# Kernel optimization log

Hardware: AMD Instinct MI355X
Metric: run time of the kernel (lower is better)

The kernel has to match this reference:

```python
import jax, jax.numpy as jnp
import numpy as np

HIDDEN_DIM = 2048
HEAD_NUM = 16
HEAD_DIM = HIDDEN_DIM // HEAD_NUM


def setup_inputs() -> dict:
    key = jax.random.key(0)
    ks = jax.random.split(key, 9)
    B, S, H = 2, 2048, HIDDEN_DIM
    scale = 1.0 / np.sqrt(H)
    X = jax.random.normal(ks[0], (B, S, H), dtype=jnp.float32)
    Wq = jax.random.normal(ks[1], (H, H), dtype=jnp.float32) * scale
    bq = jnp.zeros((H,), dtype=jnp.float32)
    Wk = jax.random.normal(ks[2], (H, H), dtype=jnp.float32) * scale
    bk = jnp.zeros((H,), dtype=jnp.float32)
    Wv = jax.random.normal(ks[3], (H, H), dtype=jnp.float32) * scale
    bv = jnp.zeros((H,), dtype=jnp.float32)
    Wo = jax.random.normal(ks[4], (H, H), dtype=jnp.float32) * scale
    bo = jnp.zeros((H,), dtype=jnp.float32)
    return {"X": X, "Wq": Wq, "bq": bq, "Wk": Wk, "bk": bk,
            "Wv": Wv, "bv": bv, "Wo": Wo, "bo": bo}


def reference(X, Wq, bq, Wk, bk, Wv, bv, Wo, bo):
    B, S, H = X.shape
    # QKV projections (nn.Linear applies x @ W.T + b; weights here stored as [in, out])
    Q = X @ Wq + bq
    K = X @ Wk + bk
    V = X @ Wv + bv
    # [B, heads, S, head_dim]
    q = Q.reshape(B, S, HEAD_NUM, HEAD_DIM).transpose(0, 2, 1, 3)
    k = K.reshape(B, S, HEAD_NUM, HEAD_DIM).transpose(0, 2, 1, 3)
    v = V.reshape(B, S, HEAD_NUM, HEAD_DIM).transpose(0, 2, 1, 3)
    scores = jnp.einsum('bhqd,bhkd->bhqk', q, k) / jnp.sqrt(jnp.float32(HEAD_DIM))
    attn = jax.nn.softmax(scores, axis=-1)  # dropout = identity in eval
    out = jnp.einsum('bhqk,bhkd->bhqd', attn, v)
    out = out.transpose(0, 2, 1, 3).reshape(B, S, H)
    return out @ Wo + bo
```

## Files before the change

kernel.cpp:

```cpp
#include <hip/hip_runtime.h>
#include <hip/hip_bf16.h>
#include <stdint.h>


#define Bc 2
#define Sc 2048
#define Hc 2048
#define NHc 16
#define Dc 128
#define Mc 4096

typedef unsigned short ushortT;
typedef float f32x4 __attribute__((ext_vector_type(4)));
typedef _Float16 f16x8 __attribute__((ext_vector_type(8)));

#define MFMAH(a, b, c) __builtin_amdgcn_mfma_f32_16x16x32_f16((a), (b), (c), 0, 0, 0)
#define MF_AB(a, b, c) MFMAH((a), (b), (c))
#define MF_BA(a, b, c) MFMAH((b), (a), (c))

static __device__ __forceinline__ ushortT f2h(float x) {
    _Float16 h = (_Float16)x;
    return __builtin_bit_cast(unsigned short, h);
}

static __device__ __forceinline__ void load_lds16(const ushortT* g, ushortT* l) {
    __builtin_amdgcn_global_load_lds(
        (__attribute__((address_space(1))) void*)(g),
        (__attribute__((address_space(3))) void*)(l), 16, 0, 0);
}

__global__ __launch_bounds__(256) void pack_a(
    const float* __restrict__ src, ushortT* __restrict__ dst)
{
    const int mt = blockIdx.x, kt = blockIdx.y;
    const int t = threadIdx.x;
    const int kq = t & 15;
    const int r0 = t >> 4;
    ushortT* tile = dst + ((size_t)(mt * 32 + kt)) * 8192;
#pragma unroll
    for (int rr = 0; rr < 8; ++rr) {
        const int row = r0 + rr * 16;
        const float4 v = *(const float4*)(src + (size_t)(mt * 128 + row) * Hc + kt * 64 + kq * 4);
        _Float16 h[4] = {(_Float16)v.x, (_Float16)v.y, (_Float16)v.z, (_Float16)v.w};
        const int gid = kq >> 1, halfg = kq & 1;
        const int gp = gid ^ (row & 7);
        *(uint2*)(tile + (size_t)row * 64 + gp * 8 + halfg * 4) = *(uint2*)h;
    }
}

__global__ __launch_bounds__(256) void pack_b(
    const float* __restrict__ W0, const float* __restrict__ W1,
    const float* __restrict__ W2, const float* __restrict__ W3,
    ushortT* __restrict__ dst)
{
    const int nt = blockIdx.x, kt = blockIdx.y, which = blockIdx.z;
    const float* W = (which == 0) ? W0 : (which == 1) ? W1 : (which == 2) ? W2 : W3;
    const int t = threadIdx.x;
    const int n0 = (t & 31) * 4;
    const int kg = t >> 5;
    ushortT* tile = dst + (size_t)which * 4194304 + ((size_t)(nt * 32 + kt)) * 8192;
    _Float16 h[4][8];
#pragma unroll
    for (int j = 0; j < 8; ++j) {
        const float4 v = *(const float4*)&W[(size_t)(kt * 64 + kg * 8 + j) * Hc + nt * 128 + n0];
        h[0][j] = (_Float16)v.x; h[1][j] = (_Float16)v.y;
        h[2][j] = (_Float16)v.z; h[3][j] = (_Float16)v.w;
    }
#pragma unroll
    for (int i = 0; i < 4; ++i) {
        const int n = n0 + i;
        *(uint4*)(tile + (size_t)n * 64 + ((kg ^ (n & 7)) << 3)) = *(uint4*)h[i];
    }
}

#define GEMM_PROLOGUE()                                                        \
    __shared__ __align__(16) ushortT As[8192], Bs[8192];                       \
    const int tid = threadIdx.x, wv_ = tid >> 6, lane = tid & 63;              \
    const int lane16 = lane & 15, quad = lane >> 4;                            \
    const int quad4 = quad * 4;                                                \
    const int wm = (wv_ & 1) * 64, wn = (wv_ >> 1) * 64;                       \
    int aoff[4][2], boff[4][2];                                                \
    _Pragma("unroll") for (int mi = 0; mi < 4; ++mi)                           \
        _Pragma("unroll") for (int kf = 0; kf < 2; ++kf) {                     \
            const int ra = wm + mi * 16 + lane16;                              \
            aoff[mi][kf] = ra * 64 + (((kf * 4 + quad) ^ (ra & 7)) << 3);      \
            const int rb = wn + mi * 16 + lane16;                              \
            boff[mi][kf] = rb * 64 + (((kf * 4 + quad) ^ (rb & 7)) << 3);      \
        }                                                                      \
    f32x4 acc[4][4];                                                           \
    _Pragma("unroll") for (int i = 0; i < 4; ++i)                              \
        _Pragma("unroll") for (int j = 0; j < 4; ++j) {                        \
            acc[i][j][0] = 0.f; acc[i][j][1] = 0.f;                            \
            acc[i][j][2] = 0.f; acc[i][j][3] = 0.f; }                          \
    ushortT* asd = &As[wv_ * 2048];                                            \
    ushortT* bsd = &Bs[wv_ * 2048];

#define GEMM_KLOOP(at, bt, MF)                                                 \
    for (int kt2 = 0; kt2 < 32; ++kt2) {                                       \
        _Pragma("unroll") for (int i = 0; i < 4; ++i) {                        \
            load_lds16(at + i * 512 + lane * 8, asd + i * 512);                \
            load_lds16(bt + i * 512 + lane * 8, bsd + i * 512);                \
        }                                                                      \
        at += 8192; bt += 8192;                                                \
        __syncthreads();                                                       \
        _Pragma("unroll") for (int kf = 0; kf < 2; ++kf) {                     \
            f16x8 a[4], b[4];                                                  \
            _Pragma("unroll") for (int mi = 0; mi < 4; ++mi)                   \
                a[mi] = *(const f16x8*)&As[aoff[mi][kf]];                      \
            _Pragma("unroll") for (int nj = 0; nj < 4; ++nj)                   \
                b[nj] = *(const f16x8*)&Bs[boff[nj][kf]];                      \
            _Pragma("unroll") for (int nj = 0; nj < 4; ++nj)                   \
                _Pragma("unroll") for (int mi = 0; mi < 4; ++mi)               \
                    acc[mi][nj] = MF(a[mi], b[nj], acc[mi][nj]);               \
        }                                                                      \
        __syncthreads();                                                       \
    }

#define G256_PROLOGUE()                                                        \
    __shared__ __align__(16) ushortT LA[2][2][8192];                           \
    __shared__ __align__(16) ushortT LB[2][2][8192];                           \
    const int tid = threadIdx.x, wv_ = tid >> 6, lane = tid & 63;              \
    const int lane16 = lane & 15, quad = lane >> 4, quad4 = (lane >> 4) * 4;   \
    const int wr = wv_ >> 2, wc = wv_ & 3;                                     \
    const ushortT* LAr = &LA[0][0][0] + wr * 8192;                             \
    const ushortT* LBr = &LB[0][0][0] + (wc >> 1) * 8192;                      \
    int oA[2][4][2], oB[4][2];                                                 \
    _Pragma("unroll") for (int h = 0; h < 2; ++h)                              \
        _Pragma("unroll") for (int mi = 0; mi < 4; ++mi)                       \
            _Pragma("unroll") for (int kf = 0; kf < 2; ++kf) {                 \
                const int r_ = h * 64 + mi * 16 + lane16;                      \
                oA[h][mi][kf] = r_ * 64 + (((kf * 4 + quad) ^ (r_ & 7)) << 3); \
            }                                                                  \
    _Pragma("unroll") for (int nj = 0; nj < 4; ++nj)                           \
        _Pragma("unroll") for (int kf = 0; kf < 2; ++kf) {                     \
            const int r_ = (wc & 1) * 64 + nj * 16 + lane16;                   \
            oB[nj][kf] = r_ * 64 + (((kf * 4 + quad) ^ (r_ & 7)) << 3);        \
        }                                                                      \
    f32x4 acc[8][4];                                                           \
    _Pragma("unroll") for (int i = 0; i < 8; ++i)                              \
        _Pragma("unroll") for (int j = 0; j < 4; ++j) {                        \
            acc[i][j][0] = 0.f; acc[i][j][1] = 0.f;                            \
            acc[i][j][2] = 0.f; acc[i][j][3] = 0.f; }

#define STAGE(SRC, STEP, DST) do {                                             \
    const ushortT* g_ = (SRC) + (size_t)(STEP) * 8192;                         \
    ushortT* l_ = (DST) + wv_ * 1024;                                          \
    load_lds16(g_, l_);                                                        \
    load_lds16(g_ + 512, l_ + 512);                                            \
} while (0)

#define RD_A03(S)                                                              \
    _Pragma("unroll") for (int mi = 0; mi < 4; ++mi)                           \
        _Pragma("unroll") for (int kf = 0; kf < 2; ++kf)                       \
            a03[mi][kf] = *(const f16x8*)&LAr[(S) * 16384 + oA[0][mi][kf]];

#define RD_A47(S)                                                              \
    _Pragma("unroll") for (int mi = 0; mi < 4; ++mi)                           \
        _Pragma("unroll") for (int kf = 0; kf < 2; ++kf)                       \
            a47[mi][kf] = *(const f16x8*)&LAr[(S) * 16384 + oA[1][mi][kf]];

#define RD_B01(S)                                                              \
    _Pragma("unroll") for (int nj = 0; nj < 2; ++nj)                           \
        _Pragma("unroll") for (int kf = 0; kf < 2; ++kf)                       \
            b[nj][kf] = *(const f16x8*)&LBr[(S) * 16384 + oB[nj][kf]];

#define RD_B23(S)                                                              \
    _Pragma("unroll") for (int nj = 2; nj < 4; ++nj)                           \
        _Pragma("unroll") for (int kf = 0; kf < 2; ++kf)                       \
            b[nj][kf] = *(const f16x8*)&LBr[(S) * 16384 + oB[nj][kf]];

#define QUADQ(ARR, MIB, NJB, MF)                                               \
    _Pragma("unroll") for (int kf = 0; kf < 2; ++kf)                           \
        _Pragma("unroll") for (int mi = 0; mi < 4; ++mi)                       \
            _Pragma("unroll") for (int nj = 0; nj < 2; ++nj)                   \
                acc[(MIB) + mi][(NJB) + nj] =                                  \
                    MF(ARR[mi][kf], b[(NJB) + nj][kf], acc[(MIB) + mi][(NJB) + nj]);

#define PRE_MFMA()                                                             \
    __builtin_amdgcn_s_barrier();                                              \
    __builtin_amdgcn_s_setprio(1);

#define POST_MFMA()                                                            \
    __builtin_amdgcn_s_setprio(0);                                             \
    __builtin_amdgcn_s_barrier();

#define VMC6() asm volatile("s_waitcnt vmcnt(6)" ::: "memory")
#define VMC4() asm volatile("s_waitcnt vmcnt(4)" ::: "memory")

#define MINS(x) ((x) < 31 ? (x) : 31)

#define G256_MAIN(AB0, AB1, BB0, BB1, MF)                                      \
    const ushortT* sA0 = (AB0) + wv_ * 1024 + lane * 8;                        \
    const ushortT* sA1 = (AB1) + wv_ * 1024 + lane * 8;                        \
    const ushortT* sB0 = (BB0) + wv_ * 1024 + lane * 8;                        \
    const ushortT* sB1 = (BB1) + wv_ * 1024 + lane * 8;                        \
      \
    STAGE(sB0, 0, &LB[0][0][0]); STAGE(sB1, 0, &LB[0][1][0]);                  \
    STAGE(sA0, 0, &LA[0][0][0]); STAGE(sA1, 0, &LA[0][1][0]);                  \
    STAGE(sB0, 1, &LB[1][0][0]); STAGE(sB1, 1, &LB[1][1][0]);                  \
    STAGE(sA0, 1, &LA[1][0][0]);                                               \
    VMC6();                                                                    \
    __builtin_amdgcn_s_barrier();                                              \
    _Pragma("clang loop unroll(disable)")                                      \
    for (int t = 0; t < 32; t += 2) {                                          \
        f16x8 a03[4][2], a47[4][2], b[4][2];                                   \
                                        \
        RD_A03(0); RD_B01(0);                                                  \
        STAGE(sA1, t + 1, &LA[1][1][0]);                                       \
        PRE_MFMA(); QUADQ(a03, 0, 0, MF); POST_MFMA();                         \
                                                       \
        RD_B23(0);                                                             \
        PRE_MFMA(); QUADQ(a03, 0, 2, MF); POST_MFMA();                         \
                             \
        RD_A47(0);                                                             \
        STAGE(sB0, MINS(t + 2), &LB[0][0][0]);                                 \
        PRE_MFMA(); QUADQ(a47, 4, 2, MF); POST_MFMA();                         \
              \
        STAGE(sB1, MINS(t + 2), &LB[0][1][0]);                                 \
        VMC4();                                                                \
        PRE_MFMA(); QUADQ(a47, 4, 0, MF); POST_MFMA();                         \
                        \
        RD_A03(1); RD_B01(1);                                                  \
        STAGE(sA0, MINS(t + 2), &LA[0][0][0]);                                 \
        STAGE(sA1, MINS(t + 2), &LA[0][1][0]);                                 \
        PRE_MFMA(); QUADQ(a03, 0, 0, MF); POST_MFMA();                         \
                                                                       \
        RD_B23(1);                                                             \
        PRE_MFMA(); QUADQ(a03, 0, 2, MF); POST_MFMA();                         \
                                                                       \
        RD_A47(1);                                                             \
        STAGE(sB0, MINS(t + 3), &LB[1][0][0]);                                 \
        PRE_MFMA(); QUADQ(a47, 4, 2, MF); POST_MFMA();                         \
        \
        STAGE(sB1, MINS(t + 3), &LB[1][1][0]);                                 \
        STAGE(sA0, MINS(t + 3), &LA[1][0][0]);                                 \
        VMC6();                                                                \
        PRE_MFMA(); QUADQ(a47, 4, 0, MF); POST_MFMA();                         \
    }

__global__ __launch_bounds__(512, 2) void qkv_gemm256(
    const ushortT* __restrict__ Xp, const ushortT* __restrict__ Wall,
    const float* __restrict__ bq, const float* __restrict__ bk,
    const float* __restrict__ bv,
    ushortT* __restrict__ Qd, ushortT* __restrict__ Kd, ushortT* __restrict__ Vt)
{
    const int id = blockIdx.x;
    const int swz = (id & 7) * 48 + (id >> 3);
    const int mt = swz & 15;
    const int bn = swz >> 4;
    const int which = bn >> 3, bnw = bn & 7;
    const ushortT* Ab0 = Xp + (size_t)((2 * mt + 0) * 32) * 8192;
    const ushortT* Ab1 = Xp + (size_t)((2 * mt + 1) * 32) * 8192;
    const ushortT* Wp  = Wall + (size_t)which * 4194304;
    const ushortT* Bb0 = Wp + (size_t)((bnw * 2 + 0) * 32) * 8192;
    const ushortT* Bb1 = Wp + (size_t)((bnw * 2 + 1) * 32) * 8192;
    const float* bias = (which == 0) ? bq : (which == 1) ? bk : bv;

    G256_PROLOGUE();

    const float QS = 0.08838834764831845f * 1.4426950408889634f;

    if (which == 2) {
        G256_MAIN(Ab0, Ab1, Bb0, Bb1, MF_AB);
        asm volatile("s_waitcnt vmcnt(0)" ::: "memory");
#pragma unroll
        for (int nj = 0; nj < 4; ++nj) {
            const int colm = bnw * 256 + wc * 64 + nj * 16 + lane16;
            const float bb2 = bias[colm];
            const int dd = colm & 127;
            const int hh = colm >> 7;
#pragma unroll
            for (int mi = 0; mi < 8; ++mi) {
                const int m0 = mt * 256 + wr * 128 + mi * 16 + quad4;
                const int b = m0 >> 11, s0_ = m0 & 2047;
                const size_t bhb = (size_t)(b * NHc + hh) * (Sc * Dc);
                const int t2 = s0_ >> 6, sin0 = s0_ & 63;
                uint2 u;
                u.x = (uint32_t)f2h(acc[mi][nj][0] + bb2) |
                      ((uint32_t)f2h(acc[mi][nj][1] + bb2) << 16);
                u.y = (uint32_t)f2h(acc[mi][nj][2] + bb2) |
                      ((uint32_t)f2h(acc[mi][nj][3] + bb2) << 16);
                *(uint2*)&Vt[bhb + (size_t)t2 * 8192 + dd * 64 +
                             (((sin0 >> 3) ^ (dd & 7)) << 3) + (sin0 & 7)] = u;
            }
        }
    } else {
        G256_MAIN(Ab0, Ab1, Bb0, Bb1, MF_BA);
        asm volatile("s_waitcnt vmcnt(0)" ::: "memory");
#pragma unroll
        for (int nj = 0; nj < 4; ++nj) {
            const int col0 = bnw * 256 + wc * 64 + nj * 16 + quad4;
            const float4 bv4 = *(const float4*)&bias[col0];
            const int dd0 = col0 & 127;
            const int hh = col0 >> 7;
#pragma unroll
            for (int mi = 0; mi < 8; ++mi) {
                const int m = mt * 256 + wr * 128 + mi * 16 + lane16;
                const int b = m >> 11, s = m & 2047;
                const size_t bhb = (size_t)(b * NHc + hh) * (Sc * Dc);
                float v0 = acc[mi][nj][0] + bv4.x;
                float v1 = acc[mi][nj][1] + bv4.y;
                float v2 = acc[mi][nj][2] + bv4.z;
                float v3 = acc[mi][nj][3] + bv4.w;
                if (which == 0) {
                    uint2 u;
                    u.x = (uint32_t)f2h(v0 * QS) | ((uint32_t)f2h(v1 * QS) << 16);
                    u.y = (uint32_t)f2h(v2 * QS) | ((uint32_t)f2h(v3 * QS) << 16);
                    *(uint2*)&Qd[bhb + (size_t)s * Dc + dd0] = u;
                } else {
                    const int t2 = s >> 6, sin_ = s & 63;
                    uint2 u;
                    u.x = (uint32_t)f2h(v0) | ((uint32_t)f2h(v1) << 16);
                    u.y = (uint32_t)f2h(v2) | ((uint32_t)f2h(v3) << 16);
                    *(uint2*)&Kd[bhb + (size_t)t2 * 8192 + sin_ * 128 +
                                 (((dd0 >> 3) ^ (sin_ & 7)) << 3) + (dd0 & 7)] = u;
                }
            }
        }
    }
}

__global__ __launch_bounds__(128, 2) void attn(
    const ushortT* __restrict__ Qd, const ushortT* __restrict__ Kt,
    const ushortT* __restrict__ Vt, ushortT* __restrict__ AOp)
{
    const int id = blockIdx.x;
    const int slot = id >> 3;
    const int pair = (id & 7) + ((slot >> 5) << 3);
    const int qt = slot & 31;
    const int hh = pair & 15, bb = pair >> 4;

    const ushortT* Qp  = Qd + ((size_t)(bb * NHc + hh)) * Sc * Dc;
    const ushortT* Kbh = Kt + ((size_t)(bb * NHc + hh)) * Sc * Dc;
    const ushortT* Vbh = Vt + ((size_t)(bb * NHc + hh)) * Sc * Dc;

    __shared__ __align__(16) ushortT Ks[8192];
    __shared__ __align__(16) ushortT Vs[8192];
    __shared__ __align__(16) ushortT Pbuf[2][2048];

    const int tid = threadIdx.x, wv_ = tid >> 6, lane = tid & 63;
    const int lane16 = lane & 15, quad = lane >> 4;
    const int quad8 = quad * 8, quad4 = quad * 4;
    const int s0 = qt * 64 + wv_ * 32;

    f16x8 q[2][4];
#pragma unroll
    for (int nj = 0; nj < 2; ++nj)
#pragma unroll
        for (int kf = 0; kf < 4; ++kf)
            q[nj][kf] = *(const f16x8*)(Qp + (size_t)(s0 + nj * 16 + lane16) * Dc + kf * 32 + quad8);

    f32x4 o[8][2];
#pragma unroll
    for (int dj = 0; dj < 8; ++dj)
#pragma unroll
        for (int nj = 0; nj < 2; ++nj) { o[dj][nj][0] = 0.f; o[dj][nj][1] = 0.f; o[dj][nj][2] = 0.f; o[dj][nj][3] = 0.f; }

    float m_run[2] = {-1e30f, -1e30f}, l_run[2] = {0.f, 0.f};
    ushortT* Pw = Pbuf[wv_];

    for (int nt = 0; nt < 32; ++nt) {
        const ushortT* ktile = Kbh + (size_t)nt * 8192 + wv_ * 4096;
        const ushortT* vtile = Vbh + (size_t)nt * 8192 + wv_ * 4096;
#pragma unroll
        for (int i = 0; i < 8; ++i) {
            load_lds16(ktile + i * 512 + lane * 8, Ks + wv_ * 4096 + i * 512);
            load_lds16(vtile + i * 512 + lane * 8, Vs + wv_ * 4096 + i * 512);
        }
        __syncthreads();

        f32x4 sacc[4][2];
#pragma unroll
        for (int mi = 0; mi < 4; ++mi)
#pragma unroll
            for (int nj = 0; nj < 2; ++nj) { sacc[mi][nj][0] = 0.f; sacc[mi][nj][1] = 0.f; sacc[mi][nj][2] = 0.f; sacc[mi][nj][3] = 0.f; }
        __builtin_amdgcn_s_setprio(1);
#pragma unroll
        for (int kf = 0; kf < 4; ++kf) {
            f16x8 kb[4];
#pragma unroll
            for (int mi = 0; mi < 4; ++mi) {
                const int row = mi * 16 + lane16;
                kb[mi] = *(const f16x8*)&Ks[row * 128 + (((kf * 4 + quad) ^ (row & 7)) << 3)];
            }
#pragma unroll
            for (int mi = 0; mi < 4; ++mi)
#pragma unroll
                for (int nj = 0; nj < 2; ++nj)
                    sacc[mi][nj] = MFMAH(kb[mi], q[nj][kf], sacc[mi][nj]);
        }
        __builtin_amdgcn_s_setprio(0);

        float alpha_[2];
#pragma unroll
        for (int nj = 0; nj < 2; ++nj) {
            float mx = sacc[0][nj][0];
#pragma unroll
            for (int mi = 0; mi < 4; ++mi)
#pragma unroll
                for (int r = 0; r < 4; ++r) mx = fmaxf(mx, sacc[mi][nj][r]);
            mx = fmaxf(mx, __shfl_xor(mx, 16));
            mx = fmaxf(mx, __shfl_xor(mx, 32));
            const float mnew = fmaxf(m_run[nj], mx);
            alpha_[nj] = exp2f(m_run[nj] - mnew);
            m_run[nj] = mnew;
            float sum = 0.f;
#pragma unroll
            for (int mi = 0; mi < 4; ++mi)
#pragma unroll
                for (int r = 0; r < 4; ++r) {
                    const float p = exp2f(sacc[mi][nj][r] - mnew);
                    sacc[mi][nj][r] = p;
                    sum += p;
                }
            sum += __shfl_xor(sum, 16);
            sum += __shfl_xor(sum, 32);
            l_run[nj] = l_run[nj] * alpha_[nj] + sum;
            const int prow = nj * 16 + lane16;
#pragma unroll
            for (int mi = 0; mi < 4; ++mi) {
                uint2 u;
                u.x = (uint32_t)f2h(sacc[mi][nj][0]) | ((uint32_t)f2h(sacc[mi][nj][1]) << 16);
                u.y = (uint32_t)f2h(sacc[mi][nj][2]) | ((uint32_t)f2h(sacc[mi][nj][3]) << 16);
                const int g = mi * 2 + (quad >> 1);
                *(uint2*)&Pw[prow * 64 + ((g ^ (prow & 7)) << 3) + (quad & 1) * 4] = u;
            }
        }

        if (__ballot((alpha_[0] != 1.f) | (alpha_[1] != 1.f)) != 0ull) {
#pragma unroll
            for (int dj = 0; dj < 8; ++dj)
#pragma unroll
                for (int nj = 0; nj < 2; ++nj) {
                    const float av = alpha_[nj];
                    o[dj][nj][0] *= av; o[dj][nj][1] *= av;
                    o[dj][nj][2] *= av; o[dj][nj][3] *= av;
                }
        }

        __builtin_amdgcn_s_setprio(1);
#pragma unroll
        for (int kf2 = 0; kf2 < 2; ++kf2) {
            f16x8 pb[2];
#pragma unroll
            for (int nj = 0; nj < 2; ++nj) {
                const int row = nj * 16 + lane16;
                pb[nj] = *(const f16x8*)&Pw[row * 64 + (((kf2 * 4 + quad) ^ (row & 7)) << 3)];
            }
#pragma unroll
            for (int dj = 0; dj < 8; ++dj) {
                const int row = dj * 16 + lane16;
                const f16x8 vb = *(const f16x8*)&Vs[row * 64 + (((kf2 * 4 + quad) ^ (row & 7)) << 3)];
#pragma unroll
                for (int nj = 0; nj < 2; ++nj)
                    o[dj][nj] = MFMAH(vb, pb[nj], o[dj][nj]);
            }
        }
        __builtin_amdgcn_s_setprio(0);
        __syncthreads();
    }

#pragma unroll
    for (int nj = 0; nj < 2; ++nj) {
        const float inv = 1.f / l_run[nj];
        const int m = bb * Sc + qt * 64 + wv_ * 32 + nj * 16 + lane16;
        const int mtile = m >> 7, rin = m & 127;
#pragma unroll
        for (int dj = 0; dj < 8; ++dj) {
            const int ktile = hh * 2 + (dj >> 2);
            const int cin0 = (dj & 3) * 16 + quad4;
            const int g = cin0 >> 3, e0 = cin0 & 7;
            uint2 u;
            u.x = (uint32_t)f2h(o[dj][nj][0] * inv) | ((uint32_t)f2h(o[dj][nj][1] * inv) << 16);
            u.y = (uint32_t)f2h(o[dj][nj][2] * inv) | ((uint32_t)f2h(o[dj][nj][3] * inv) << 16);
            *(uint2*)&AOp[((size_t)(mtile * 32 + ktile)) * 8192 + rin * 64 +
                          ((g ^ (rin & 7)) << 3) + e0] = u;
        }
    }
}

__global__ __launch_bounds__(256) void out_gemm(
    const ushortT* __restrict__ AOp, const ushortT* __restrict__ Wop,
    const float* __restrict__ bo, float* __restrict__ out)
{
    const int nt = blockIdx.x;
    const int mt = blockIdx.y;

    GEMM_PROLOGUE();

    const ushortT* at = AOp + (size_t)(mt * 32) * 8192 + wv_ * 2048;
    const ushortT* bt = Wop + (size_t)(nt * 32) * 8192 + wv_ * 2048;
    GEMM_KLOOP(at, bt, MF_BA);

#pragma unroll
    for (int nj = 0; nj < 4; ++nj) {
        const int col0 = nt * 128 + wn + nj * 16 + quad4;
        const float4 bv4 = *(const float4*)&bo[col0];
#pragma unroll
        for (int mi = 0; mi < 4; ++mi) {
            const int m = mt * 128 + wm + mi * 16 + lane16;
            float4 v;
            v.x = acc[mi][nj][0] + bv4.x;
            v.y = acc[mi][nj][1] + bv4.y;
            v.z = acc[mi][nj][2] + bv4.z;
            v.w = acc[mi][nj][3] + bv4.w;
            *(float4*)&out[(size_t)m * Hc + col0] = v;
        }
    }
}

extern "C" void kernel_launch(void* const* d_in, const int* in_sizes, int n_in,
                              void* d_out, int out_size, void* d_ws, size_t ws_size,
                              hipStream_t stream) {
    (void)in_sizes; (void)n_in; (void)out_size; (void)ws_size;

    const float* X  = (const float*)d_in[0];
    const float* Wq = (const float*)d_in[1];
    const float* bq = (const float*)d_in[2];
    const float* Wk = (const float*)d_in[3];
    const float* bk = (const float*)d_in[4];
    const float* Wv = (const float*)d_in[5];
    const float* bv = (const float*)d_in[6];
    const float* Wo = (const float*)d_in[7];
    const float* bo = (const float*)d_in[8];
    float* out = (float*)d_out;

    ushortT* ws = (ushortT*)d_ws;
    const size_t E = (size_t)Mc * Hc;
    const size_t WE = (size_t)Hc * Hc;
    ushortT* Xp   = ws;
    ushortT* Wall = Xp + E;
    ushortT* Qd   = Wall + 4 * WE;
    ushortT* Kd   = Qd + E;
    ushortT* Vtp  = Kd + E;
    ushortT* AOp  = Vtp + E;

    pack_a<<<dim3(32, 32), 256, 0, stream>>>(X, Xp);
    pack_b<<<dim3(16, 32, 4), 256, 0, stream>>>(Wq, Wk, Wv, Wo, Wall);
    qkv_gemm256<<<dim3(384), 512, 0, stream>>>(Xp, Wall, bq, bk, bv, Qd, Kd, Vtp);
    attn<<<dim3(1024), 128, 0, stream>>>(Qd, Kd, Vtp, AOp);
    out_gemm<<<dim3(16, 32), 256, 0, stream>>>(AOp, Wall + 3 * WE, bo, out);
}
```

Measured before the change: 430.2 us.

## Double-buffer K/V tiles in attention and widen blocks to 128 queries

The attention kernel now runs 4 waves (256 threads) per block covering 128 query rows, so each K/V tile staged in LDS is shared by twice as many queries. K/V tiles are double-buffered, with the next tile prefetched while the current one is computed on, to hide global-to-LDS latency. The grid is halved and the block-to-XCD mapping is changed so each XCD handles a group of heads. LDS use roughly doubles (about 80KB per block), which may limit how many blocks fit per CU.

```diff
diff --git a/kernel.cpp b/kernel.cpp
--- a/kernel.cpp
+++ b/kernel.cpp
@@ -194,7 +194,6 @@
     const ushortT* sA1 = (AB1) + wv_ * 1024 + lane * 8;                        \
     const ushortT* sB0 = (BB0) + wv_ * 1024 + lane * 8;                        \
     const ushortT* sB1 = (BB1) + wv_ * 1024 + lane * 8;                        \
-      \
     STAGE(sB0, 0, &LB[0][0][0]); STAGE(sB1, 0, &LB[0][1][0]);                  \
     STAGE(sA0, 0, &LA[0][0][0]); STAGE(sA1, 0, &LA[0][1][0]);                  \
     STAGE(sB0, 1, &LB[1][0][0]); STAGE(sB1, 1, &LB[1][1][0]);                  \
@@ -211,15 +210,15 @@
                                                        \
         RD_B23(0);                                                             \
         PRE_MFMA(); QUADQ(a03, 0, 2, MF); POST_MFMA();                         \
-                             \
+                                                       \
         RD_A47(0);                                                             \
         STAGE(sB0, MINS(t + 2), &LB[0][0][0]);                                 \
         PRE_MFMA(); QUADQ(a47, 4, 2, MF); POST_MFMA();                         \
-              \
+                              \
         STAGE(sB1, MINS(t + 2), &LB[0][1][0]);                                 \
         VMC4();                                                                \
         PRE_MFMA(); QUADQ(a47, 4, 0, MF); POST_MFMA();                         \
-                        \
+                                                     \
         RD_A03(1); RD_B01(1);                                                  \
         STAGE(sA0, MINS(t + 2), &LA[0][0][0]);                                 \
         STAGE(sA1, MINS(t + 2), &LA[0][1][0]);                                 \
@@ -231,7 +230,7 @@
         RD_A47(1);                                                             \
         STAGE(sB0, MINS(t + 3), &LB[1][0][0]);                                 \
         PRE_MFMA(); QUADQ(a47, 4, 2, MF); POST_MFMA();                         \
-        \
+                          \
         STAGE(sB1, MINS(t + 3), &LB[1][1][0]);                                 \
         STAGE(sA0, MINS(t + 3), &LA[1][0][0]);                                 \
         VMC6();                                                                \
@@ -320,28 +319,29 @@
     }
 }
 
-__global__ __launch_bounds__(128, 2) void attn(
+__global__ __launch_bounds__(256, 2) void attn(
     const ushortT* __restrict__ Qd, const ushortT* __restrict__ Kt,
     const ushortT* __restrict__ Vt, ushortT* __restrict__ AOp)
 {
     const int id = blockIdx.x;
-    const int slot = id >> 3;
-    const int pair = (id & 7) + ((slot >> 5) << 3);
-    const int qt = slot & 31;
+    const int xcd = id & 7;
+    const int idx = id >> 3;
+    const int pair = (xcd << 2) | (idx >> 4);
+    const int qt = idx & 15;
     const int hh = pair & 15, bb = pair >> 4;
 
     const ushortT* Qp  = Qd + ((size_t)(bb * NHc + hh)) * Sc * Dc;
     const ushortT* Kbh = Kt + ((size_t)(bb * NHc + hh)) * Sc * Dc;
     const ushortT* Vbh = Vt + ((size_t)(bb * NHc + hh)) * Sc * Dc;
 
-    __shared__ __align__(16) ushortT Ks[8192];
-    __shared__ __align__(16) ushortT Vs[8192];
-    __shared__ __align__(16) ushortT Pbuf[2][2048];
+    __shared__ __align__(16) ushortT Ks[2][8192];
+    __shared__ __align__(16) ushortT Vs[2][8192];
+    __shared__ __align__(16) ushortT Pbuf[4][2048];
 
     const int tid = threadIdx.x, wv_ = tid >> 6, lane = tid & 63;
     const int lane16 = lane & 15, quad = lane >> 4;
     const int quad8 = quad * 8, quad4 = quad * 4;
-    const int s0 = qt * 64 + wv_ * 32;
+    const int s0 = qt * 128 + wv_ * 32;
 
     f16x8 q[2][4];
 #pragma unroll
@@ -359,15 +359,23 @@
     float m_run[2] = {-1e30f, -1e30f}, l_run[2] = {0.f, 0.f};
     ushortT* Pw = Pbuf[wv_];
 
+#define ASTAGE(NT, SLOT) do {                                                  \
+        const ushortT* kt_ = Kbh + (size_t)(NT) * 8192 + wv_ * 2048 + lane * 8;\
+        const ushortT* vt_ = Vbh + (size_t)(NT) * 8192 + wv_ * 2048 + lane * 8;\
+        _Pragma("unroll") for (int i = 0; i < 4; ++i) {                        \
+            load_lds16(kt_ + i * 512, &Ks[SLOT][wv_ * 2048 + i * 512]);        \
+            load_lds16(vt_ + i * 512, &Vs[SLOT][wv_ * 2048 + i * 512]);        \
+        }                                                                      \
+    } while (0)
+
+    ASTAGE(0, 0);
+    __syncthreads();
+    int cur = 0;
+
     for (int nt = 0; nt < 32; ++nt) {
-        const ushortT* ktile = Kbh + (size_t)nt * 8192 + wv_ * 4096;
-        const ushortT* vtile = Vbh + (size_t)nt * 8192 + wv_ * 4096;
-#pragma unroll
-        for (int i = 0; i < 8; ++i) {
-            load_lds16(ktile + i * 512 + lane * 8, Ks + wv_ * 4096 + i * 512);
-            load_lds16(vtile + i * 512 + lane * 8, Vs + wv_ * 4096 + i * 512);
-        }
-        __syncthreads();
+        if (nt + 1 < 32) ASTAGE(nt + 1, cur ^ 1);
+        const ushortT* Ksc = Ks[cur];
+        const ushortT* Vsc = Vs[cur];
 
         f32x4 sacc[4][2];
 #pragma unroll
@@ -381,7 +389,7 @@
 #pragma unroll
             for (int mi = 0; mi < 4; ++mi) {
                 const int row = mi * 16 + lane16;
-                kb[mi] = *(const f16x8*)&Ks[row * 128 + (((kf * 4 + quad) ^ (row & 7)) << 3)];
+                kb[mi] = *(const f16x8*)&Ksc[row * 128 + (((kf * 4 + quad) ^ (row & 7)) << 3)];
             }
 #pragma unroll
             for (int mi = 0; mi < 4; ++mi)
@@ -450,7 +458,7 @@
 #pragma unroll
             for (int dj = 0; dj < 8; ++dj) {
                 const int row = dj * 16 + lane16;
-                const f16x8 vb = *(const f16x8*)&Vs[row * 64 + (((kf2 * 4 + quad) ^ (row & 7)) << 3)];
+                const f16x8 vb = *(const f16x8*)&Vsc[row * 64 + (((kf2 * 4 + quad) ^ (row & 7)) << 3)];
 #pragma unroll
                 for (int nj = 0; nj < 2; ++nj)
                     o[dj][nj] = MFMAH(vb, pb[nj], o[dj][nj]);
@@ -458,12 +466,13 @@
         }
         __builtin_amdgcn_s_setprio(0);
         __syncthreads();
+        cur ^= 1;
     }
 
 #pragma unroll
     for (int nj = 0; nj < 2; ++nj) {
         const float inv = 1.f / l_run[nj];
-        const int m = bb * Sc + qt * 64 + wv_ * 32 + nj * 16 + lane16;
+        const int m = bb * Sc + qt * 128 + wv_ * 32 + nj * 16 + lane16;
         const int mtile = m >> 7, rin = m & 127;
 #pragma unroll
         for (int dj = 0; dj < 8; ++dj) {
@@ -477,6 +486,7 @@
                           ((g ^ (rin & 7)) << 3) + e0] = u;
         }
     }
+#undef ASTAGE
 }
 
 __global__ __launch_bounds__(256) void out_gemm(
@@ -538,6 +548,6 @@
     pack_a<<<dim3(32, 32), 256, 0, stream>>>(X, Xp);
     pack_b<<<dim3(16, 32, 4), 256, 0, stream>>>(Wq, Wk, Wv, Wo, Wall);
     qkv_gemm256<<<dim3(384), 512, 0, stream>>>(Xp, Wall, bq, bk, bv, Qd, Kd, Vtp);
-    attn<<<dim3(1024), 128, 0, stream>>>(Qd, Kd, Vtp, AOp);
+    attn<<<dim3(512), 256, 0, stream>>>(Qd, Kd, Vtp, AOp);
     out_gemm<<<dim3(16, 32), 256, 0, stream>>>(AOp, Wall + 3 * WE, bo, out);
 }
```

After: 431.4 us. No clear change (+0.3%).
